# Performance work log

Measured on AMD Instinct MI355X. Metric: run time of the kernel, lower is better.

Reference implementation:

```python
import jax, jax.numpy as jnp
import numpy as np

EPS = 1e-6
TEMP_GEO = 0.07
W_LOCAL = 0.5
W_SHARP = 0.5


def _l2norm(x):
    return x / jnp.clip(jnp.linalg.norm(x, axis=-1, keepdims=True), 1e-12)


def setup_inputs() -> dict:
    key = jax.random.key(0)
    ks = jax.random.split(key, 6)
    B, L, S, C = 8, 1024, 1024, 128
    N, P = 8, 256
    q_geo = _l2norm(jax.random.normal(ks[0], (B, L, C), jnp.float32))
    geo_pos = _l2norm(jax.random.normal(ks[1], (B, S, C), jnp.float32))
    label = jax.random.randint(ks[2], (B, L, S), 0, 2, jnp.int32)
    q_cl = jax.random.normal(ks[3], (N, P, C), jnp.float32)
    cl_pos = jax.random.normal(ks[4], (N, P, C), jnp.float32)
    idx = jax.random.randint(ks[5], (N,), 0, P, jnp.int32)
    return {"q_geo": q_geo, "q_cl": q_cl, "geo_pos": geo_pos,
            "cl_pos": cl_pos, "label": label, "idx": idx}


def _masked_mean(v, m):
    # per-sample mean over the [L,S] plane of entries where m is True
    m = m.astype(v.dtype)
    return jnp.sum(v * m, axis=(1, 2)) / jnp.maximum(jnp.sum(m, axis=(1, 2)), 1.0)


def _loftr_loss(conf, label):
    # standard LoFTR coarse CE loss (LoFTRLoss source absent from repo snippet)
    conf = jnp.clip(conf, EPS, 1.0 - EPS)
    pos = label == 1
    neg = label == 0
    pos_loss = _masked_mean(-jnp.log(conf), pos)          # [B]
    neg_loss = _masked_mean(-jnp.log(1.0 - conf), neg)    # [B]
    loss = pos_loss + neg_loss
    return jnp.mean(loss), jnp.mean(pos_loss), jnp.mean(neg_loss)


def _geometric_loss(q, k, label):
    sim = jnp.einsum('blc,bsc->bls', q, k) / TEMP_GEO        # [B,L,S]
    conf = jax.nn.softmax(sim, axis=1) * jax.nn.softmax(sim, axis=2)
    return _loftr_loss(conf, label)


def _sharpness_loss(q, k, label):
    sim = (1.0 + jnp.einsum('blc,bsc->bls', q, k)) / 2.0     # [B,L,S]
    # column stats (over L, dim=0 per sample) -> sharpness1 [B,S]
    s1 = (jnp.max(sim, axis=1) - jnp.mean(sim, axis=1)) / jnp.std(sim, axis=1, ddof=1)
    sharp1 = jax.nn.softmax(s1, axis=-1)
    # row stats (over S, dim=1 per sample) -> sharpness2 [B,L]
    s2 = (jnp.max(sim, axis=2) - jnp.mean(sim, axis=2)) / jnp.std(sim, axis=2, ddof=1)
    sharp2 = jax.nn.softmax(s2, axis=-1)
    simc = jnp.clip(sim, EPS, 1.0 - EPS)
    nll = -jnp.log(simc)
    pos = (label == 1).astype(simc.dtype)
    neg = (label == 0)
    loss1 = jnp.sum(nll * sharp1[:, None, :] * pos, axis=(1, 2))   # [B]
    loss2 = jnp.sum(nll * sharp2[:, :, None] * pos, axis=(1, 2))   # [B]
    loss3 = _masked_mean(-jnp.log(1.0 - simc), neg)                # [B]
    losses = (loss1 + loss2) / 2.0 + loss3
    return sharp1, jnp.mean(losses)


def _contrast_loss(q, all_k):
    # intended math of GeCoContrast: full cosine matrix, diag positives, tail negatives
    N = q.shape[0]
    sim = (1.0 + _l2norm(q) @ _l2norm(all_k).T) / 2.0   # [N, M]
    sim = jnp.clip(sim, EPS, 1.0 - EPS)
    l_pos = jnp.diagonal(sim[:, :N])                    # [N]
    l_neg = sim[:, N:]                                  # [N, M-N]
    return (jnp.mean(-jnp.log(l_pos)) + jnp.mean(-jnp.log(1.0 - l_neg))) / 2.0


def _forward(q_geo, q_cl, geo_pos, cl_pos, label, idx):
    loss_geo, geo_pos_loss, geo_neg_loss = _geometric_loss(q_geo, geo_pos, label)
    sharpness, loss_sharp = _sharpness_loss(q_geo, geo_pos, label)
    loss_geo = ((1.0 - W_SHARP) * loss_geo + W_SHARP * loss_sharp) * W_LOCAL

    N, P, C = q_cl.shape
    ar = jnp.arange(N)
    q_sel = q_cl[ar, idx]                               # [N,C]
    sel = cl_pos[ar, idx]                               # [N,C] positives moved to slot 0
    first = cl_pos[:, 0, :]
    swapped = cl_pos.at[ar, idx].set(first).at[:, 0, :].set(sel)
    cl_pos_save = sel
    all_k = jnp.concatenate([swapped[:, 0, :],
                             swapped[:, 1:, :].reshape(N * (P - 1), C)], axis=0)
    loss_cl = _contrast_loss(q_sel, all_k) * (1.0 - W_LOCAL)

    total = loss_geo + loss_cl
    return (sharpness, cl_pos_save, total, geo_pos_loss, geo_neg_loss, loss_sharp, loss_cl)


def reference(q_geo, q_cl, geo_pos, cl_pos, label, idx):
    return _forward(q_geo, q_cl, geo_pos, cl_pos, label, idx)
```

## Files before the change

kernel.cpp:

```cpp
#include <hip/hip_runtime.h>
#include <math.h>

#define BB 8
#define LL 1024
#define SS 1024
#define CC 128
#define NN 8
#define PP 256

static constexpr float EPS       = 1e-6f;
static constexpr float ONE_M_EPS = 1.0f - 1e-6f;
static constexpr float INV_T     = 1.0f / 0.07f;
static constexpr float NLL_MAX   = 13.815511f;
static constexpr float NLL_MIN   = 1.0000005e-6f;

static constexpr size_t DOTSZ      = (size_t)BB * LL * SS;
static constexpr size_t OFF_LSER   = DOTSZ;
static constexpr size_t OFF_S2RAW  = DOTSZ + 8192;
static constexpr size_t OFF_LSEC   = DOTSZ + 16384;
static constexpr size_t OFF_S1RAW  = DOTSZ + 24576;
static constexpr size_t OFF_SHARP2 = DOTSZ + 32768;
static constexpr int    LCH        = 16;
static constexpr size_t OFF_COLP   = DOTSZ + 40960;
static constexpr size_t OFF_ACC    = OFF_COLP + (size_t)BB * LCH * 4 * SS;
static constexpr size_t OFF_ACCCL  = OFF_ACC + 48;
static constexpr size_t OFF_QN     = OFF_ACC + 64;

static constexpr int OUT_CLSAVE = 8192;
static constexpr int OUT_SCAL   = 9216;

typedef __bf16 bf16x8 __attribute__((ext_vector_type(8)));
typedef float  floatx4 __attribute__((ext_vector_type(4)));

__device__ __forceinline__ void split_bf16(float x, short& hi, short& lo) {
    unsigned u = __builtin_bit_cast(unsigned, x);
    unsigned r = (u + 0x7FFFu + ((u >> 16) & 1u)) & 0xFFFF0000u;
    hi = (short)(r >> 16);
    float res = x - __builtin_bit_cast(float, r);
    unsigned u2 = __builtin_bit_cast(unsigned, res);
    lo = (short)((u2 + 0x7FFFu + ((u2 >> 16) & 1u)) >> 16);
}

__global__ __launch_bounds__(512) void prep(const float* __restrict__ q_cl,
                                            const float* __restrict__ cl_pos,
                                            const int* __restrict__ idx,
                                            float* __restrict__ out, float* __restrict__ ws) {
    int tid = threadIdx.x;
    if (tid < 50) ws[OFF_ACC + tid] = 0.0f;
    int n = tid >> 6, lane = tid & 63;
    int in = idx[n];
    const float* q = q_cl + ((size_t)(n * PP + in)) * CC;
    float2 qv = *(const float2*)(q + 2 * lane);
    float ss = qv.x * qv.x + qv.y * qv.y;
    for (int o = 32; o; o >>= 1) ss += __shfl_xor(ss, o);
    float inv = 1.0f / fmaxf(sqrtf(ss), 1e-12f);
    *(float2*)(ws + OFF_QN + n * 128 + 2 * lane) = make_float2(qv.x * inv, qv.y * inv);
    const float* cp = cl_pos + ((size_t)(n * PP + in)) * CC;
    float2 cv = *(const float2*)(cp + 2 * lane);
    *(float2*)(out + OUT_CLSAVE + n * 128 + 2 * lane) = cv;
}

__global__ __launch_bounds__(256) void gemm_dot(const float* __restrict__ A,
                                                const float* __restrict__ Bm,
                                                float* __restrict__ dot) {
    int b  = blockIdx.z;
    int l0 = blockIdx.y * 128;
    int s0 = blockIdx.x * 128;
    __shared__ short Ah[128 * 32];
    __shared__ short Al[128 * 32];
    __shared__ short Bh[128 * 32];
    __shared__ short Bl[128 * 32];

    int tid  = threadIdx.x;
    int lane = tid & 63;
    int w    = tid >> 6;
    int wr   = (w >> 1) * 64;
    int wc   = (w & 1) * 64;
    int fl   = lane & 15;
    int quad = lane >> 4;

    const float* Ab = A  + ((size_t)b * LL + l0) * CC;
    const float* Bb = Bm + ((size_t)b * SS + s0) * CC;

    floatx4 acc[4][4];
#pragma unroll
    for (int i = 0; i < 4; i++)
#pragma unroll
        for (int j = 0; j < 4; j++) acc[i][j] = (floatx4){0.f, 0.f, 0.f, 0.f};

    for (int c0 = 0; c0 < 128; c0 += 32) {
        if (c0) __syncthreads();
#pragma unroll
        for (int rep = 0; rep < 4; rep++) {
            int slot = tid + rep * 256;
            int row  = slot >> 3;
            int c4   = (slot & 7) * 4;
            float4 a4 = *(const float4*)(Ab + (size_t)row * CC + c0 + c4);
            float4 b4 = *(const float4*)(Bb + (size_t)row * CC + c0 + c4);
            short4 ah, al, bh, bl;
            split_bf16(a4.x, ah.x, al.x); split_bf16(a4.y, ah.y, al.y);
            split_bf16(a4.z, ah.z, al.z); split_bf16(a4.w, ah.w, al.w);
            split_bf16(b4.x, bh.x, bl.x); split_bf16(b4.y, bh.y, bl.y);
            split_bf16(b4.z, bh.z, bl.z); split_bf16(b4.w, bh.w, bl.w);
            int off = row * 32 + c4;
            *(short4*)(Ah + off) = ah; *(short4*)(Al + off) = al;
            *(short4*)(Bh + off) = bh; *(short4*)(Bl + off) = bl;
        }
        __syncthreads();

        bf16x8 afh[4], afl[4];
#pragma unroll
        for (int mt = 0; mt < 4; mt++) {
            int off = (wr + mt * 16 + fl) * 32 + quad * 8;
            afh[mt] = *reinterpret_cast<const bf16x8*>(Ah + off);
            afl[mt] = *reinterpret_cast<const bf16x8*>(Al + off);
        }
#pragma unroll
        for (int nt = 0; nt < 4; nt++) {
            int off = (wc + nt * 16 + fl) * 32 + quad * 8;
            bf16x8 bfh = *reinterpret_cast<const bf16x8*>(Bh + off);
            bf16x8 bfl = *reinterpret_cast<const bf16x8*>(Bl + off);
#pragma unroll
            for (int mt = 0; mt < 4; mt++) {
                acc[mt][nt] = __builtin_amdgcn_mfma_f32_16x16x32_bf16(afh[mt], bfh, acc[mt][nt], 0, 0, 0);
                acc[mt][nt] = __builtin_amdgcn_mfma_f32_16x16x32_bf16(afh[mt], bfl, acc[mt][nt], 0, 0, 0);
                acc[mt][nt] = __builtin_amdgcn_mfma_f32_16x16x32_bf16(afl[mt], bfh, acc[mt][nt], 0, 0, 0);
            }
        }
    }

    float* D = dot + ((size_t)b * LL + l0) * SS + s0;
#pragma unroll
    for (int mt = 0; mt < 4; mt++)
#pragma unroll
        for (int nt = 0; nt < 4; nt++) {
            int col = wc + nt * 16 + fl;
#pragma unroll
            for (int r = 0; r < 4; r++) {
                int row = wr + mt * 16 + quad * 4 + r;
                D[(size_t)row * SS + col] = acc[mt][nt][r];
            }
        }
}

__global__ __launch_bounds__(256) void row_stats(const float* __restrict__ dot, float* __restrict__ ws) {
    int row = blockIdx.x;
    const float4* p = (const float4*)(dot + (size_t)row * SS);
    float4 v = p[threadIdx.x];
    float vals[4] = {v.x, v.y, v.z, v.w};
    float es = 0.0f, mx = -1e30f, sm = 0.0f, sq = 0.0f;
#pragma unroll
    for (int j = 0; j < 4; j++) {
        float d = vals[j];
        es += __expf(d * INV_T);
        float s2 = 0.5f + 0.5f * d;
        mx = fmaxf(mx, s2);
        sm += s2;
        sq += s2 * s2;
    }
    for (int o = 32; o; o >>= 1) {
        es += __shfl_xor(es, o);
        mx = fmaxf(mx, __shfl_xor(mx, o));
        sm += __shfl_xor(sm, o);
        sq += __shfl_xor(sq, o);
    }
    __shared__ float sb[4][4];
    int lane = threadIdx.x & 63, wid = threadIdx.x >> 6;
    if (!lane) { sb[0][wid] = es; sb[1][wid] = mx; sb[2][wid] = sm; sb[3][wid] = sq; }
    __syncthreads();
    if (threadIdx.x == 0) {
        es = sb[0][0] + sb[0][1] + sb[0][2] + sb[0][3];
        mx = fmaxf(fmaxf(sb[1][0], sb[1][1]), fmaxf(sb[1][2], sb[1][3]));
        sm = sb[2][0] + sb[2][1] + sb[2][2] + sb[2][3];
        sq = sb[3][0] + sb[3][1] + sb[3][2] + sb[3][3];
        ws[OFF_LSER + row] = __logf(es);
        float mean = sm * (1.0f / SS);
        float var = (sq - sm * sm * (1.0f / SS)) * (1.0f / (SS - 1));
        ws[OFF_S2RAW + row] = (mx - mean) / sqrtf(fmaxf(var, 1e-30f));
    }
}

__global__ __launch_bounds__(256) void col_part(const float* __restrict__ dot, float* __restrict__ ws) {
    int b = blockIdx.z, lc = blockIdx.y, sc = blockIdx.x;
    int s = sc * 256 + threadIdx.x;
    const float* base = dot + ((size_t)(b * LL + lc * (LL / LCH))) * SS + s;
    float es = 0.0f, mx = -1e30f, sm = 0.0f, sq = 0.0f;
    for (int l = 0; l < LL / LCH; l++) {
        float d = base[(size_t)l * SS];
        es += __expf(d * INV_T);
        float s2 = 0.5f + 0.5f * d;
        mx = fmaxf(mx, s2);
        sm += s2;
        sq += s2 * s2;
    }
    float* cp = ws + OFF_COLP + ((size_t)(b * LCH + lc) * 4) * SS + s;
    cp[0] = es; cp[SS] = mx; cp[2 * SS] = sm; cp[3 * SS] = sq;
}

__global__ __launch_bounds__(256) void col_combine(float* __restrict__ ws) {
    int b = blockIdx.y, sc = blockIdx.x;
    int s = sc * 256 + threadIdx.x;
    float es = 0.0f, mx = -1e30f, sm = 0.0f, sq = 0.0f;
    for (int lc = 0; lc < LCH; lc++) {
        const float* cp = ws + OFF_COLP + ((size_t)(b * LCH + lc) * 4) * SS + s;
        es += cp[0];
        mx = fmaxf(mx, cp[SS]);
        sm += cp[2 * SS];
        sq += cp[3 * SS];
    }
    ws[OFF_LSEC + (size_t)b * SS + s] = __logf(es);
    float mean = sm * (1.0f / LL);
    float var = (sq - sm * sm * (1.0f / LL)) * (1.0f / (LL - 1));
    ws[OFF_S1RAW + (size_t)b * SS + s] = (mx - mean) / sqrtf(fmaxf(var, 1e-30f));
}

__global__ __launch_bounds__(256) void softmax16(float* __restrict__ ws, float* __restrict__ out) {
    int q = blockIdx.x;
    int b = q & 7;
    const float* src = ws + ((q < 8) ? OFF_S1RAW : OFF_S2RAW) + (size_t)b * 1024;
    float* dst = (q < 8) ? (out + (size_t)b * 1024) : (ws + OFF_SHARP2 + (size_t)b * 1024);
    float4 v = ((const float4*)src)[threadIdx.x];
    int lane = threadIdx.x & 63, wid = threadIdx.x >> 6;
    __shared__ float sb[4];
    __shared__ float red;
    float mx = fmaxf(fmaxf(v.x, v.y), fmaxf(v.z, v.w));
    for (int o = 32; o; o >>= 1) mx = fmaxf(mx, __shfl_xor(mx, o));
    if (!lane) sb[wid] = mx;
    __syncthreads();
    if (threadIdx.x == 0) red = fmaxf(fmaxf(sb[0], sb[1]), fmaxf(sb[2], sb[3]));
    __syncthreads();
    mx = red;
    float e0 = __expf(v.x - mx), e1 = __expf(v.y - mx), e2 = __expf(v.z - mx), e3 = __expf(v.w - mx);
    float sm = e0 + e1 + e2 + e3;
    for (int o = 32; o; o >>= 1) sm += __shfl_xor(sm, o);
    __syncthreads();
    if (!lane) sb[wid] = sm;
    __syncthreads();
    if (threadIdx.x == 0) red = sb[0] + sb[1] + sb[2] + sb[3];
    __syncthreads();
    float inv = 1.0f / red;
    ((float4*)dst)[threadIdx.x] = make_float4(e0 * inv, e1 * inv, e2 * inv, e3 * inv);
}

__device__ __forceinline__ void proc_elem(float d, int lab, float lcj, float sh1j,
                                          float lr, float s2v,
                                          float& posg, float& negg, float& l1, float& l2,
                                          float& negs, float& pcf) {
    float t = lr + lcj - d * (2.0f * INV_T);
    float isPos = (lab == 1) ? 1.0f : 0.0f;
    float isNeg = 1.0f - isPos;
    float tp   = fminf(fmaxf(t, NLL_MIN), NLL_MAX);
    float simc = fminf(fmaxf(fmaf(0.5f, d, 0.5f), EPS), ONE_M_EPS);
    float om   = fminf(fmaxf(fmaf(-0.5f, d, 0.5f), EPS), ONE_M_EPS);
    float nll2 = -__logf(simc);
    float cf   = fminf(fmaxf(__expf(-t), EPS), ONE_M_EPS);
    float nllg = -__logf(1.0f - cf);
    float nlls = -__logf(om);
    posg += isPos * tp;
    l1   += isPos * nll2 * sh1j;
    l2   += isPos * nll2 * s2v;
    pcf  += isPos;
    negg += isNeg * nllg;
    negs += isNeg * nlls;
}

__global__ __launch_bounds__(256) void main_loss(const float* __restrict__ dot,
                                                 const int* __restrict__ label,
                                                 const float* __restrict__ sharp1,
                                                 float* __restrict__ ws) {
    int b = blockIdx.y;
    int l0 = blockIdx.x * 4;
    int s = threadIdx.x * 4;
    float4 lc4 = *(const float4*)(ws + OFF_LSEC + (size_t)b * 1024 + s);
    float4 sh1 = *(const float4*)(sharp1 + (size_t)b * 1024 + s);
    const float* lser = ws + OFF_LSER + (size_t)b * 1024;
    const float* sh2  = ws + OFF_SHARP2 + (size_t)b * 1024;
    float posg = 0, negg = 0, l1 = 0, l2 = 0, negs = 0, pcf = 0;
#pragma unroll
    for (int r = 0; r < 4; r++) {
        int l = l0 + r;
        float lr  = lser[l];
        float s2v = sh2[l];
        size_t base = ((size_t)(b * 1024 + l)) * 1024 + s;
        float4 d4 = *(const float4*)(dot + base);
        int4  lb  = *(const int4*)(label + base);
        proc_elem(d4.x, lb.x, lc4.x, sh1.x, lr, s2v, posg, negg, l1, l2, negs, pcf);
        proc_elem(d4.y, lb.y, lc4.y, sh1.y, lr, s2v, posg, negg, l1, l2, negs, pcf);
        proc_elem(d4.z, lb.z, lc4.z, sh1.z, lr, s2v, posg, negg, l1, l2, negs, pcf);
        proc_elem(d4.w, lb.w, lc4.w, sh1.w, lr, s2v, posg, negg, l1, l2, negs, pcf);
    }
    float vals[6] = {posg, negg, l1, l2, negs, pcf};
    __shared__ float sb[6][4];
    int lane = threadIdx.x & 63, wid = threadIdx.x >> 6;
#pragma unroll
    for (int k = 0; k < 6; k++) {
        float v = vals[k];
        for (int o = 32; o; o >>= 1) v += __shfl_xor(v, o);
        if (!lane) sb[k][wid] = v;
    }
    __syncthreads();
    if (threadIdx.x < 6) {
        float r = sb[threadIdx.x][0] + sb[threadIdx.x][1] + sb[threadIdx.x][2] + sb[threadIdx.x][3];
        atomicAdd(ws + OFF_ACC + (size_t)b * 6 + threadIdx.x, r);
    }
}

__global__ __launch_bounds__(256) void contrast(const float* __restrict__ cl_pos,
                                                const int* __restrict__ idx,
                                                float* __restrict__ ws) {
    int j = blockIdx.x * 4 + (threadIdx.x >> 6);
    int lane = threadIdx.x & 63;
    int m, p;
    if (j < NN) {
        m = j; p = idx[j];
    } else {
        int jj = j - NN;
        m = jj / (PP - 1);
        p = 1 + (jj - m * (PP - 1));
        if (p == idx[m]) p = 0;
    }
    const float* k = cl_pos + ((size_t)(m * PP + p)) * CC;
    float2 kv = *(const float2*)(k + 2 * lane);
    float ksq = kv.x * kv.x + kv.y * kv.y;
    for (int o = 32; o; o >>= 1) ksq += __shfl_xor(ksq, o);
    float invkn = 1.0f / fmaxf(sqrtf(ksq), 1e-12f);
    float pos = 0.0f, neg = 0.0f;
    if (j < NN) {
        const float2 qv = *(const float2*)(ws + OFF_QN + j * 128 + 2 * lane);
        float dt = qv.x * kv.x + qv.y * kv.y;
        for (int o = 32; o; o >>= 1) dt += __shfl_xor(dt, o);
        float sim = fminf(fmaxf(fmaf(0.5f * invkn, dt, 0.5f), EPS), ONE_M_EPS);
        pos = -__logf(sim);
    } else {
#pragma unroll
        for (int n = 0; n < NN; n++) {
            const float2 qv = *(const float2*)(ws + OFF_QN + n * 128 + 2 * lane);
            float dt = qv.x * kv.x + qv.y * kv.y;
            for (int o = 32; o; o >>= 1) dt += __shfl_xor(dt, o);
            float om = fminf(fmaxf(fmaf(-0.5f * invkn, dt, 0.5f), EPS), ONE_M_EPS);
            neg -= __logf(om);
        }
    }
    __shared__ float sb[2][4];
    int w = threadIdx.x >> 6;
    if (!lane) { sb[0][w] = pos; sb[1][w] = neg; }
    __syncthreads();
    if (threadIdx.x == 0) {
        float ps = sb[0][0] + sb[0][1] + sb[0][2] + sb[0][3];
        float ng = sb[1][0] + sb[1][1] + sb[1][2] + sb[1][3];
        if (ps != 0.0f) atomicAdd(ws + OFF_ACCCL + 0, ps);
        if (ng != 0.0f) atomicAdd(ws + OFF_ACCCL + 1, ng);
    }
}

__global__ void finalize(float* __restrict__ out, const float* __restrict__ ws) {
    if (threadIdx.x != 0) return;
    float gp = 0, gn = 0, lsh = 0;
    for (int b = 0; b < 8; b++) {
        const float* a = ws + OFF_ACC + (size_t)b * 6;
        float pc = a[5];
        float nc = (float)((size_t)LL * SS) - pc;
        gp += a[0] / fmaxf(pc, 1.0f);
        gn += a[1] / fmaxf(nc, 1.0f);
        lsh += (a[2] + a[3]) * 0.5f + a[4] / fmaxf(nc, 1.0f);
    }
    gp *= 0.125f; gn *= 0.125f; lsh *= 0.125f;
    float lgeo = gp + gn;
    float lgw = (0.5f * lgeo + 0.5f * lsh) * 0.5f;
    float clp = ws[OFF_ACCCL + 0] / 8.0f;
    float cln = ws[OFF_ACCCL + 1] / (8.0f * 2040.0f);
    float lcl = (clp + cln) * 0.5f * 0.5f;
    out[OUT_SCAL + 0] = lgw + lcl;
    out[OUT_SCAL + 1] = gp;
    out[OUT_SCAL + 2] = gn;
    out[OUT_SCAL + 3] = lsh;
    out[OUT_SCAL + 4] = lcl;
}

extern "C" void kernel_launch(void* const* d_in, const int* in_sizes, int n_in,
                              void* d_out, int out_size, void* d_ws, size_t ws_size,
                              hipStream_t stream) {
    const float* q_geo   = (const float*)d_in[0];
    const float* q_cl    = (const float*)d_in[1];
    const float* geo_pos = (const float*)d_in[2];
    const float* cl_pos  = (const float*)d_in[3];
    const int*   label   = (const int*)d_in[4];
    const int*   idx     = (const int*)d_in[5];
    float* out = (float*)d_out;
    float* ws  = (float*)d_ws;
    float* dot = ws;

    prep<<<dim3(1), dim3(512), 0, stream>>>(q_cl, cl_pos, idx, out, ws);
    gemm_dot<<<dim3(8, 8, 8), dim3(256), 0, stream>>>(q_geo, geo_pos, dot);
    row_stats<<<dim3(8192), dim3(256), 0, stream>>>(dot, ws);
    col_part<<<dim3(4, LCH, 8), dim3(256), 0, stream>>>(dot, ws);
    col_combine<<<dim3(4, 8), dim3(256), 0, stream>>>(ws);
    softmax16<<<dim3(16), dim3(256), 0, stream>>>(ws, out);
    main_loss<<<dim3(256, 8), dim3(256), 0, stream>>>(dot, label, out, ws);
    contrast<<<dim3(512), dim3(256), 0, stream>>>(cl_pos, idx, ws);
    finalize<<<dim3(1), dim3(64), 0, stream>>>(out, ws);
}
```

Measured before the change: 169.4 us.

## Fuse row/column stats into GEMM epilogue and pad LDS stride

Result: no change. 167.5 us (-1.1%).

```diff
diff --git a/kernel.cpp b/kernel.cpp
--- a/kernel.cpp
+++ b/kernel.cpp
@@ -20,9 +20,9 @@
 static constexpr size_t OFF_LSEC   = DOTSZ + 16384;
 static constexpr size_t OFF_S1RAW  = DOTSZ + 24576;
 static constexpr size_t OFF_SHARP2 = DOTSZ + 32768;
-static constexpr int    LCH        = 16;
-static constexpr size_t OFF_COLP   = DOTSZ + 40960;
-static constexpr size_t OFF_ACC    = OFF_COLP + (size_t)BB * LCH * 4 * SS;
+static constexpr size_t OFF_RP     = DOTSZ + 40960;
+static constexpr size_t OFF_CP     = OFF_RP + 262144;
+static constexpr size_t OFF_ACC    = OFF_RP + 524288;
 static constexpr size_t OFF_ACCCL  = OFF_ACC + 48;
 static constexpr size_t OFF_QN     = OFF_ACC + 64;
 
@@ -31,6 +31,8 @@
 
 typedef __bf16 bf16x8 __attribute__((ext_vector_type(8)));
 typedef float  floatx4 __attribute__((ext_vector_type(4)));
+
+#define LSTR 40
 
 __device__ __forceinline__ void split_bf16(float x, short& hi, short& lo) {
     unsigned u = __builtin_bit_cast(unsigned, x);
@@ -62,14 +64,19 @@
 
 __global__ __launch_bounds__(256) void gemm_dot(const float* __restrict__ A,
                                                 const float* __restrict__ Bm,
-                                                float* __restrict__ dot) {
+                                                float* __restrict__ dot,
+                                                float* __restrict__ ws) {
     int b  = blockIdx.z;
-    int l0 = blockIdx.y * 128;
-    int s0 = blockIdx.x * 128;
-    __shared__ short Ah[128 * 32];
-    __shared__ short Al[128 * 32];
-    __shared__ short Bh[128 * 32];
-    __shared__ short Bl[128 * 32];
+    int lt = blockIdx.y;
+    int st = blockIdx.x;
+    int l0 = lt * 128;
+    int s0 = st * 128;
+    __shared__ short Ah[128 * LSTR];
+    __shared__ short Al[128 * LSTR];
+    __shared__ short Bh[128 * LSTR];
+    __shared__ short Bl[128 * LSTR];
+    __shared__ float rowLDS[2][128][4];
+    __shared__ float colLDS[2][128][4];
 
     int tid  = threadIdx.x;
     int lane = tid & 63;
@@ -102,7 +109,7 @@
             split_bf16(a4.z, ah.z, al.z); split_bf16(a4.w, ah.w, al.w);
             split_bf16(b4.x, bh.x, bl.x); split_bf16(b4.y, bh.y, bl.y);
             split_bf16(b4.z, bh.z, bl.z); split_bf16(b4.w, bh.w, bl.w);
-            int off = row * 32 + c4;
+            int off = row * LSTR + c4;
             *(short4*)(Ah + off) = ah; *(short4*)(Al + off) = al;
             *(short4*)(Bh + off) = bh; *(short4*)(Bl + off) = bl;
         }
@@ -111,13 +118,13 @@
         bf16x8 afh[4], afl[4];
 #pragma unroll
         for (int mt = 0; mt < 4; mt++) {
-            int off = (wr + mt * 16 + fl) * 32 + quad * 8;
+            int off = (wr + mt * 16 + fl) * LSTR + quad * 8;
             afh[mt] = *reinterpret_cast<const bf16x8*>(Ah + off);
             afl[mt] = *reinterpret_cast<const bf16x8*>(Al + off);
         }
 #pragma unroll
         for (int nt = 0; nt < 4; nt++) {
-            int off = (wc + nt * 16 + fl) * 32 + quad * 8;
+            int off = (wc + nt * 16 + fl) * LSTR + quad * 8;
             bf16x8 bfh = *reinterpret_cast<const bf16x8*>(Bh + off);
             bf16x8 bfl = *reinterpret_cast<const bf16x8*>(Bl + off);
 #pragma unroll
@@ -141,77 +148,92 @@
                 D[(size_t)row * SS + col] = acc[mt][nt][r];
             }
         }
-}
-
-__global__ __launch_bounds__(256) void row_stats(const float* __restrict__ dot, float* __restrict__ ws) {
-    int row = blockIdx.x;
-    const float4* p = (const float4*)(dot + (size_t)row * SS);
-    float4 v = p[threadIdx.x];
-    float vals[4] = {v.x, v.y, v.z, v.w};
-    float es = 0.0f, mx = -1e30f, sm = 0.0f, sq = 0.0f;
-#pragma unroll
-    for (int j = 0; j < 4; j++) {
-        float d = vals[j];
-        es += __expf(d * INV_T);
-        float s2 = 0.5f + 0.5f * d;
-        mx = fmaxf(mx, s2);
-        sm += s2;
-        sq += s2 * s2;
-    }
-    for (int o = 32; o; o >>= 1) {
-        es += __shfl_xor(es, o);
-        mx = fmaxf(mx, __shfl_xor(mx, o));
-        sm += __shfl_xor(sm, o);
-        sq += __shfl_xor(sq, o);
-    }
-    __shared__ float sb[4][4];
-    int lane = threadIdx.x & 63, wid = threadIdx.x >> 6;
-    if (!lane) { sb[0][wid] = es; sb[1][wid] = mx; sb[2][wid] = sm; sb[3][wid] = sq; }
-    __syncthreads();
-    if (threadIdx.x == 0) {
-        es = sb[0][0] + sb[0][1] + sb[0][2] + sb[0][3];
-        mx = fmaxf(fmaxf(sb[1][0], sb[1][1]), fmaxf(sb[1][2], sb[1][3]));
-        sm = sb[2][0] + sb[2][1] + sb[2][2] + sb[2][3];
-        sq = sb[3][0] + sb[3][1] + sb[3][2] + sb[3][3];
-        ws[OFF_LSER + row] = __logf(es);
-        float mean = sm * (1.0f / SS);
-        float var = (sq - sm * sm * (1.0f / SS)) * (1.0f / (SS - 1));
-        ws[OFF_S2RAW + row] = (mx - mean) / sqrtf(fmaxf(var, 1e-30f));
-    }
-}
-
-__global__ __launch_bounds__(256) void col_part(const float* __restrict__ dot, float* __restrict__ ws) {
-    int b = blockIdx.z, lc = blockIdx.y, sc = blockIdx.x;
-    int s = sc * 256 + threadIdx.x;
-    const float* base = dot + ((size_t)(b * LL + lc * (LL / LCH))) * SS + s;
-    float es = 0.0f, mx = -1e30f, sm = 0.0f, sq = 0.0f;
-    for (int l = 0; l < LL / LCH; l++) {
-        float d = base[(size_t)l * SS];
-        es += __expf(d * INV_T);
-        float s2 = 0.5f + 0.5f * d;
-        mx = fmaxf(mx, s2);
-        sm += s2;
-        sq += s2 * s2;
-    }
-    float* cp = ws + OFF_COLP + ((size_t)(b * LCH + lc) * 4) * SS + s;
-    cp[0] = es; cp[SS] = mx; cp[2 * SS] = sm; cp[3 * SS] = sq;
-}
-
-__global__ __launch_bounds__(256) void col_combine(float* __restrict__ ws) {
-    int b = blockIdx.y, sc = blockIdx.x;
-    int s = sc * 256 + threadIdx.x;
-    float es = 0.0f, mx = -1e30f, sm = 0.0f, sq = 0.0f;
-    for (int lc = 0; lc < LCH; lc++) {
-        const float* cp = ws + OFF_COLP + ((size_t)(b * LCH + lc) * 4) * SS + s;
-        es += cp[0];
-        mx = fmaxf(mx, cp[SS]);
-        sm += cp[2 * SS];
-        sq += cp[3 * SS];
-    }
-    ws[OFF_LSEC + (size_t)b * SS + s] = __logf(es);
-    float mean = sm * (1.0f / LL);
-    float var = (sq - sm * sm * (1.0f / LL)) * (1.0f / (LL - 1));
-    ws[OFF_S1RAW + (size_t)b * SS + s] = (mx - mean) / sqrtf(fmaxf(var, 1e-30f));
+
+    float ces[4], cmx[4], csm[4], csq[4];
+#pragma unroll
+    for (int nt = 0; nt < 4; nt++) { ces[nt] = 0.f; cmx[nt] = -1e30f; csm[nt] = 0.f; csq[nt] = 0.f; }
+#pragma unroll
+    for (int mt = 0; mt < 4; mt++) {
+#pragma unroll
+        for (int r = 0; r < 4; r++) {
+            float es = 0.f, mx = -1e30f, sm = 0.f, sq = 0.f;
+#pragma unroll
+            for (int nt = 0; nt < 4; nt++) {
+                float d  = acc[mt][nt][r];
+                float e  = __expf(d * INV_T);
+                float s2 = fmaf(0.5f, d, 0.5f);
+                es += e; mx = fmaxf(mx, s2); sm += s2; sq += s2 * s2;
+                ces[nt] += e; cmx[nt] = fmaxf(cmx[nt], s2); csm[nt] += s2; csq[nt] += s2 * s2;
+            }
+            for (int o = 1; o < 16; o <<= 1) {
+                es += __shfl_xor(es, o);
+                mx = fmaxf(mx, __shfl_xor(mx, o));
+                sm += __shfl_xor(sm, o);
+                sq += __shfl_xor(sq, o);
+            }
+            if (fl == 0) {
+                int rib = wr + mt * 16 + quad * 4 + r;
+                rowLDS[w & 1][rib][0] = es; rowLDS[w & 1][rib][1] = mx;
+                rowLDS[w & 1][rib][2] = sm; rowLDS[w & 1][rib][3] = sq;
+            }
+        }
+    }
+#pragma unroll
+    for (int nt = 0; nt < 4; nt++) {
+        float es = ces[nt], mx = cmx[nt], sm = csm[nt], sq = csq[nt];
+        for (int o = 16; o < 64; o <<= 1) {
+            es += __shfl_xor(es, o);
+            mx = fmaxf(mx, __shfl_xor(mx, o));
+            sm += __shfl_xor(sm, o);
+            sq += __shfl_xor(sq, o);
+        }
+        if (quad == 0) {
+            int cib = wc + nt * 16 + fl;
+            colLDS[w >> 1][cib][0] = es; colLDS[w >> 1][cib][1] = mx;
+            colLDS[w >> 1][cib][2] = sm; colLDS[w >> 1][cib][3] = sq;
+        }
+    }
+    __syncthreads();
+    if (tid < 128) {
+        int rr = tid;
+        float es = rowLDS[0][rr][0] + rowLDS[1][rr][0];
+        float mx = fmaxf(rowLDS[0][rr][1], rowLDS[1][rr][1]);
+        float sm = rowLDS[0][rr][2] + rowLDS[1][rr][2];
+        float sq = rowLDS[0][rr][3] + rowLDS[1][rr][3];
+        float4 v = make_float4(es, mx, sm, sq);
+        *(float4*)(ws + OFF_RP + (((size_t)(b * 8 + st)) * 1024 + l0 + rr) * 4) = v;
+    } else {
+        int cc = tid - 128;
+        float es = colLDS[0][cc][0] + colLDS[1][cc][0];
+        float mx = fmaxf(colLDS[0][cc][1], colLDS[1][cc][1]);
+        float sm = colLDS[0][cc][2] + colLDS[1][cc][2];
+        float sq = colLDS[0][cc][3] + colLDS[1][cc][3];
+        float4 v = make_float4(es, mx, sm, sq);
+        *(float4*)(ws + OFF_CP + (((size_t)(b * 8 + lt)) * 1024 + s0 + cc) * 4) = v;
+    }
+}
+
+__global__ __launch_bounds__(256) void rc_combine(float* __restrict__ ws) {
+    int g = (blockIdx.x & 31) * 256 + threadIdx.x;
+    bool docol = blockIdx.x >= 32;
+    int b = g >> 10, i = g & 1023;
+    const float* part = ws + (docol ? OFF_CP : OFF_RP);
+    float es = 0.f, mx = -1e30f, sm = 0.f, sq = 0.f;
+#pragma unroll
+    for (int t = 0; t < 8; t++) {
+        float4 v = *(const float4*)(part + (((size_t)(b * 8 + t)) * 1024 + i) * 4);
+        es += v.x; mx = fmaxf(mx, v.y); sm += v.z; sq += v.w;
+    }
+    float mean = sm * (1.0f / 1024.0f);
+    float var  = (sq - sm * sm * (1.0f / 1024.0f)) * (1.0f / 1023.0f);
+    float zs   = (mx - mean) / sqrtf(fmaxf(var, 1e-30f));
+    if (!docol) {
+        ws[OFF_LSER + g]  = __logf(es);
+        ws[OFF_S2RAW + g] = zs;
+    } else {
+        ws[OFF_LSEC + g]  = __logf(es);
+        ws[OFF_S1RAW + g] = zs;
+    }
 }
 
 __global__ __launch_bounds__(256) void softmax16(float* __restrict__ ws, float* __restrict__ out) {
@@ -391,10 +413,8 @@
     float* dot = ws;
 
     prep<<<dim3(1), dim3(512), 0, stream>>>(q_cl, cl_pos, idx, out, ws);
-    gemm_dot<<<dim3(8, 8, 8), dim3(256), 0, stream>>>(q_geo, geo_pos, dot);
-    row_stats<<<dim3(8192), dim3(256), 0, stream>>>(dot, ws);
-    col_part<<<dim3(4, LCH, 8), dim3(256), 0, stream>>>(dot, ws);
-    col_combine<<<dim3(4, 8), dim3(256), 0, stream>>>(ws);
+    gemm_dot<<<dim3(8, 8, 8), dim3(256), 0, stream>>>(q_geo, geo_pos, dot, ws);
+    rc_combine<<<dim3(64), dim3(256), 0, stream>>>(ws);
     softmax16<<<dim3(16), dim3(256), 0, stream>>>(ws, out);
     main_loss<<<dim3(256, 8), dim3(256), 0, stream>>>(dot, label, out, ws);
     contrast<<<dim3(512), dim3(256), 0, stream>>>(cl_pos, idx, ws);
```
